# Performance work log

Hardware: AMD Instinct MI355X
Metric: run time of the kernel (lower is better)

## Reference

```python
import math
import jax, jax.numpy as jnp
import numpy as np

B, SENTS, L, S, D, DH, K = 128, 2, 2, 256, 1024, 64, 8
SCALE = math.sqrt(DH)
EPS = 1e-8


def gelu(x):
    return 0.5 * x * (1.0 + jax.lax.erf(x / np.float32(math.sqrt(2.0))))


def setup_inputs() -> dict:
    key = jax.random.key(0)
    ks = jax.random.split(key, 18)
    w = lambda k, shp: (jax.random.normal(k, shp, jnp.float32) * 0.02)
    return {
        "token": jax.random.normal(ks[0], (B, SENTS, L, S, D), jnp.float32),
        "kw_idx": jax.random.randint(ks[1], (B, SENTS, K), 0, S),
        "q_w": w(ks[2], (DH, D)), "q_b": jnp.zeros((DH,), jnp.float32),
        "k_w": w(ks[3], (DH, D)), "k_b": jnp.zeros((DH,), jnp.float32),
        "v_w": w(ks[4], (DH, D)), "v_b": jnp.zeros((DH,), jnp.float32),
        "mi_w": w(ks[5], (DH, D)), "mi_b": jnp.zeros((DH,), jnp.float32),
        "inter_w": w(ks[6], (4, DH, DH)), "inter_b": jnp.zeros((4, DH), jnp.float32),
        "fc0_w": w(ks[7], (64, 516)), "fc0_b": jnp.zeros((64,), jnp.float32),
        "fc1_w": w(ks[8], (2, 64)), "fc1_b": jnp.zeros((2,), jnp.float32),
    }


def _cosine(a, b):
    # torch.cosine_similarity semantics with eps=1e-8 (clamp each norm)
    na = jnp.maximum(jnp.linalg.norm(a, axis=1), EPS)
    nb = jnp.maximum(jnp.linalg.norm(b, axis=1), EPS)
    return jnp.sum(a * b, axis=1) / (na * nb)


def reference(token, kw_idx, q_w, q_b, k_w, k_b, v_w, v_b,
              mi_w, mi_b, inter_w, inter_b, fc0_w, fc0_b, fc1_w, fc1_b):
    b, _, l, s, d = token.shape
    kk = kw_idx.shape[-1]
    # faithful quirk: sent_id indexes keyword_idx[batch][sent_id - 1] -> swap sentences
    idx = kw_idx[:, ::-1, :]  # [B,2,K]
    # ragged gather (fixed K here): [B,2,L,K,D]
    kw = jnp.take_along_axis(token, idx[:, :, None, :, None], axis=3)
    kmax = kw.max(axis=3)   # [B,2,L,D]
    kavg = kw.mean(axis=3)  # [B,2,L,D]
    kw_flat = kw.reshape(b, 2, l * kk, d)  # layers concatenated along token axis

    q = jnp.einsum('bsnd,hd->bsnh', kw_flat, q_w) + q_b
    k = jnp.einsum('bsnd,hd->bsnh', kw_flat, k_w) + k_b
    v = jnp.einsum('bsnd,hd->bsnh', kw_flat, v_w) + v_b

    # cross-sentence attention WITHOUT softmax (as in original)
    att1 = jnp.einsum('bnh,bmh->bnm', q[:, 0], k[:, 1]) / SCALE
    e1 = jnp.einsum('bnm,bmh->bnh', att1, v[:, 1])  # [B,N,DH]
    att2 = jnp.einsum('bnh,bmh->bnm', q[:, 1], k[:, 0]) / SCALE
    e2 = jnp.einsum('bnm,bmh->bnh', att2, v[:, 0])
    att_feat = jnp.concatenate(
        [e1.max(axis=1), e1.mean(axis=1), e2.max(axis=1), e2.mean(axis=1)], axis=1)  # [B,4*DH]

    proj = lambda x: x @ mi_w.T + mi_b  # [B,D] -> [B,DH]
    s1_max = proj(kmax[:, 0].max(axis=1))
    s2_max = proj(kmax[:, 1].max(axis=1))
    s1_avg = proj(kavg[:, 0].mean(axis=1))
    s2_avg = proj(kavg[:, 1].mean(axis=1))

    inter = lambda i, x: x @ inter_w[i].T + inter_b[i]
    cos = jnp.stack([
        _cosine(inter(0, s1_max), s2_max),
        _cosine(inter(1, s1_max), s2_avg),
        _cosine(inter(2, s1_avg), s2_max),
        _cosine(inter(3, s1_avg), s2_avg),
    ], axis=1)  # [B,4]

    feature = jnp.concatenate([att_feat, cos, s1_max, s1_avg, s2_max, s2_avg], axis=1)  # [B,516]
    h = gelu(feature @ fc0_w.T + fc0_b)
    h = gelu(h @ fc1_w.T + fc1_b)
    return jax.nn.softmax(h, axis=-1)
```

## Files before the change

kernel.cpp:

```cpp
#include <hip/hip_runtime.h>
#include <math.h>

using short8 = __attribute__((ext_vector_type(8))) short;
using f32x4  = __attribute__((ext_vector_type(4))) float;

__device__ __forceinline__ short f2bf(float f) {
  union { float f; unsigned u; } cv; cv.f = f;
  unsigned u = cv.u;
  unsigned r = u + 0x7fffu + ((u >> 16) & 1u);
  return (short)(r >> 16);
}

__device__ __forceinline__ float gelu_f(float x) {
  return 0.5f * x * (1.0f + erff(x * 0.7071067811865475f));
}

__global__ void k_prep(const float* __restrict__ qw, const float* __restrict__ kw,
                       const float* __restrict__ vw, const float* __restrict__ miw,
                       const float* __restrict__ qb, const float* __restrict__ kb,
                       const float* __restrict__ vb, const float* __restrict__ mib,
                       short* __restrict__ Wb, float* __restrict__ biasc) {
  int t = blockIdx.x * 256 + threadIdx.x;
  int e = t * 4;
  int which = e >> 16;
  int off = e & 65535;
  const float* src = which == 0 ? qw : which == 1 ? kw : which == 2 ? vw : miw;
  float4 f = *reinterpret_cast<const float4*>(src + off);
  short s4[4] = { f2bf(f.x), f2bf(f.y), f2bf(f.z), f2bf(f.w) };
  *reinterpret_cast<unsigned long long*>(Wb + e) =
      *reinterpret_cast<unsigned long long*>(s4);
  if (blockIdx.x == 0) {
    int w = threadIdx.x >> 6, h = threadIdx.x & 63;
    const float* bsrc = w == 0 ? qb : w == 1 ? kb : w == 2 ? vb : mib;
    biasc[threadIdx.x] = bsrc[h];
  }
}

__global__ __launch_bounds__(256) void k_main(
    const float* __restrict__ token, const int* __restrict__ kwidx,
    const short* __restrict__ Wb, const float* __restrict__ biasc,
    float* __restrict__ qkv, float* __restrict__ svec) {
  constexpr int AS = 1032;
  __shared__ short A[18 * AS];
  const int bs = blockIdx.x;
  const int b = bs >> 1, snt = bs & 1;
  const int t = threadIdx.x;
  const int col = t * 4;
  const int* idxp = kwidx + (b * 2 + (1 - snt)) * 8;

  float mx[4], sm[4];
  #pragma unroll 4
  for (int i = 0; i < 16; ++i) {
    const int l = i >> 3, j = i & 7;
    const int sidx = idxp[j];
    const float4 f = *reinterpret_cast<const float4*>(
        token + (size_t)((bs * 2 + l) * 256 + sidx) * 1024 + col);
    float fv[4] = { f.x, f.y, f.z, f.w };
    short s4[4];
    #pragma unroll
    for (int c = 0; c < 4; ++c) {
      if (i == 0) { mx[c] = fv[c]; sm[c] = fv[c]; }
      else { mx[c] = fmaxf(mx[c], fv[c]); sm[c] += fv[c]; }
      s4[c] = f2bf(fv[c]);
    }
    *reinterpret_cast<unsigned long long*>(&A[i * AS + col]) =
        *reinterpret_cast<unsigned long long*>(s4);
  }
  {
    short pm4[4], pa4[4];
    #pragma unroll
    for (int c = 0; c < 4; ++c) { pm4[c] = f2bf(mx[c]); pa4[c] = f2bf(sm[c] * 0.0625f); }
    *reinterpret_cast<unsigned long long*>(&A[16 * AS + col]) =
        *reinterpret_cast<unsigned long long*>(pm4);
    *reinterpret_cast<unsigned long long*>(&A[17 * AS + col]) =
        *reinterpret_cast<unsigned long long*>(pa4);
  }
  __syncthreads();

  const int wave = t >> 6, lane = t & 63;
  const int quad = lane >> 4, mrow = lane & 15;
  const short* Abase = (wave == 3) ? &A[(16 + (mrow & 1)) * AS] : &A[mrow * AS];
  const short* w0 = Wb + (size_t)(wave * 64 + mrow) * 1024;

  f32x4 acc[4];
  #pragma unroll
  for (int i = 0; i < 4; ++i)
    #pragma unroll
    for (int r = 0; r < 4; ++r) acc[i][r] = 0.f;

  #pragma unroll 4
  for (int ko = 0; ko < 1024; ko += 32) {
    const int k0 = ko + quad * 8;
    short8 af = *reinterpret_cast<const short8*>(Abase + k0);
    short8 b0 = *reinterpret_cast<const short8*>(w0 + k0);
    short8 b1 = *reinterpret_cast<const short8*>(w0 + 16 * 1024 + k0);
    short8 b2 = *reinterpret_cast<const short8*>(w0 + 32 * 1024 + k0);
    short8 b3 = *reinterpret_cast<const short8*>(w0 + 48 * 1024 + k0);
    acc[0] = __builtin_amdgcn_mfma_f32_16x16x32_bf16(af, b0, acc[0], 0, 0, 0);
    acc[1] = __builtin_amdgcn_mfma_f32_16x16x32_bf16(af, b1, acc[1], 0, 0, 0);
    acc[2] = __builtin_amdgcn_mfma_f32_16x16x32_bf16(af, b2, acc[2], 0, 0, 0);
    acc[3] = __builtin_amdgcn_mfma_f32_16x16x32_bf16(af, b3, acc[3], 0, 0, 0);
  }

  const int row0 = quad * 4;
  #pragma unroll
  for (int i = 0; i < 4; ++i) {
    const int T = wave * 4 + i;
    const int hg = T * 16 + mrow;
    const float bias = biasc[hg];
    if (T < 12) {
      const int mat = hg >> 6, h = hg & 63;
      float* dst = qkv + ((size_t)(bs * 3 + mat) << 10) + h;
      #pragma unroll
      for (int r = 0; r < 4; ++r) dst[(row0 + r) * 64] = acc[i][r] + bias;
    } else {
      const int h = hg - 192;
      #pragma unroll
      for (int r = 0; r < 4; ++r) {
        const int n = row0 + r;
        if (n < 2) svec[(bs * 2 + n) * 64 + h] = acc[i][r] + bias;
      }
    }
  }
}

__global__ __launch_bounds__(256) void k_tail(
    const float* __restrict__ qkv, const float* __restrict__ svec,
    const float* __restrict__ interw, const float* __restrict__ interb,
    const float* __restrict__ fc0w, const float* __restrict__ fc0b,
    const float* __restrict__ fc1w, const float* __restrict__ fc1b,
    float* __restrict__ out) {
  const int b = blockIdx.x, t = threadIdx.x;
  __shared__ float qk[96 * 65];
  __shared__ float attL[256];
  __shared__ float eL[2][1024];
  __shared__ float feat[516];
  __shared__ float yv[256];
  __shared__ float hmid[64];
  __shared__ float red[256];

  const float* src = qkv + (size_t)b * 6144;
  for (int i = t; i < 6144; i += 256) {
    int row = i >> 6, h = i & 63;
    qk[row * 65 + h] = src[i];
  }
  feat[260 + t] = svec[b * 256 + t];
  __syncthreads();

  {
    const int n = t >> 4, m = t & 15;
    const float* qrow = &qk[n * 65];
    const float* krow = &qk[(64 + m) * 65];
    float acc = 0.f;
    for (int h = 0; h < 64; ++h) acc += qrow[h] * krow[h];
    attL[n * 16 + m] = acc * 0.125f;
  }
  __syncthreads();
  {
    const int h = t & 63, ng = t >> 6;
    for (int rep = 0; rep < 4; ++rep) {
      const int n = rep * 4 + ng;
      float acc = 0.f;
      #pragma unroll
      for (int m = 0; m < 16; ++m) acc += attL[n * 16 + m] * qk[(80 + m) * 65 + h];
      eL[0][n * 64 + h] = acc;
    }
  }
  __syncthreads();
  {
    const int n = t >> 4, m = t & 15;
    const float* qrow = &qk[(48 + n) * 65];
    const float* krow = &qk[(16 + m) * 65];
    float acc = 0.f;
    for (int h = 0; h < 64; ++h) acc += qrow[h] * krow[h];
    attL[n * 16 + m] = acc * 0.125f;
  }
  __syncthreads();
  {
    const int h = t & 63, ng = t >> 6;
    for (int rep = 0; rep < 4; ++rep) {
      const int n = rep * 4 + ng;
      float acc = 0.f;
      #pragma unroll
      for (int m = 0; m < 16; ++m) acc += attL[n * 16 + m] * qk[(32 + m) * 65 + h];
      eL[1][n * 64 + h] = acc;
    }
  }
  __syncthreads();
  {
    const int stat = t >> 6, h = t & 63;
    const float* ee = eL[stat >> 1];
    float r;
    if ((stat & 1) == 0) {
      r = -INFINITY;
      for (int n = 0; n < 16; ++n) r = fmaxf(r, ee[n * 64 + h]);
    } else {
      r = 0.f;
      for (int n = 0; n < 16; ++n) r += ee[n * 64 + h];
      r *= (1.f / 16.f);
    }
    feat[stat * 64 + h] = r;
  }
  __syncthreads();
  {
    const int i = t >> 6, h = t & 63;
    const float* x = (i < 2) ? &feat[260] : &feat[324];
    const float* wrow = interw + (i * 64 + h) * 64;
    float acc = interb[i * 64 + h];
    for (int hp = 0; hp < 64; ++hp) acc += x[hp] * wrow[hp];
    yv[i * 64 + h] = acc;
  }
  __syncthreads();
  if (t < 4) {
    const float* y = &yv[t * 64];
    const float* z = (t & 1) ? &feat[452] : &feat[388];
    float dy = 0.f, ny = 0.f, nz = 0.f;
    for (int h = 0; h < 64; ++h) { dy += y[h] * z[h]; ny += y[h] * y[h]; nz += z[h] * z[h]; }
    float na = fmaxf(sqrtf(ny), 1e-8f), nb = fmaxf(sqrtf(nz), 1e-8f);
    feat[256 + t] = dy / (na * nb);
  }
  __syncthreads();
  {
    const int o = t & 63, part = t >> 6;
    const int f0 = part * 129;
    const float* wrow = fc0w + o * 516;
    float acc = 0.f;
    for (int f = f0; f < f0 + 129; ++f) acc += feat[f] * wrow[f];
    red[t] = acc;
  }
  __syncthreads();
  if (t < 64) {
    float acc = fc0b[t] + red[t] + red[64 + t] + red[128 + t] + red[192 + t];
    hmid[t] = gelu_f(acc);
  }
  __syncthreads();
  if (t == 0) {
    float lg[2];
    for (int c = 0; c < 2; ++c) {
      float acc = fc1b[c];
      for (int o = 0; o < 64; ++o) acc += hmid[o] * fc1w[c * 64 + o];
      lg[c] = gelu_f(acc);
    }
    const float mxv = fmaxf(lg[0], lg[1]);
    const float e0 = expf(lg[0] - mxv), e1v = expf(lg[1] - mxv);
    out[b * 2]     = e0 / (e0 + e1v);
    out[b * 2 + 1] = e1v / (e0 + e1v);
  }
}

extern "C" void kernel_launch(void* const* d_in, const int* in_sizes, int n_in,
                              void* d_out, int out_size, void* d_ws, size_t ws_size,
                              hipStream_t stream) {
  (void)in_sizes; (void)n_in; (void)out_size; (void)ws_size;
  const float* token  = (const float*)d_in[0];
  const int*   kwidx  = (const int*)d_in[1];
  const float* qw     = (const float*)d_in[2];
  const float* qb     = (const float*)d_in[3];
  const float* kw     = (const float*)d_in[4];
  const float* kb     = (const float*)d_in[5];
  const float* vw     = (const float*)d_in[6];
  const float* vb     = (const float*)d_in[7];
  const float* miw    = (const float*)d_in[8];
  const float* mib    = (const float*)d_in[9];
  const float* interw = (const float*)d_in[10];
  const float* interb = (const float*)d_in[11];
  const float* fc0w   = (const float*)d_in[12];
  const float* fc0b   = (const float*)d_in[13];
  const float* fc1w   = (const float*)d_in[14];
  const float* fc1b   = (const float*)d_in[15];
  float* out = (float*)d_out;

  char* ws = (char*)d_ws;
  short* Wb    = (short*)(ws);
  float* biasc = (float*)(ws + 524288);
  float* qkv   = (float*)(ws + 525312);
  float* svec  = (float*)(ws + 3671040);

  k_prep<<<256, 256, 0, stream>>>(qw, kw, vw, miw, qb, kb, vb, mib, Wb, biasc);
  k_main<<<256, 256, 0, stream>>>(token, kwidx, Wb, biasc, qkv, svec);
  k_tail<<<128, 256, 0, stream>>>(qkv, svec, interw, interb, fc0w, fc0b, fc1w, fc1b, out);
}
```

Baseline: 629.4 us.

## Quadruple k_main threads with one MFMA tile per wave; coalesce tail matvecs

k_main now launches 1024 threads per block. The keyword-row gather is split across four row groups, and each of the 16 waves computes a single 16-column MFMA output tile instead of four. The goal is more memory and compute parallelism per block, since the grid has only 256 blocks. Max and mean are now computed from the bf16-rounded values held in shared memory, which slightly changes numerics and adds a barrier. In k_tail, the inter projection and fc0 layers are rewritten so lanes read weight rows contiguously and reduce with wave shuffles, replacing strided per-thread row reads.

Result: slower. 676.7 us (+7.5%).

```diff
diff --git a/kernel.cpp b/kernel.cpp
--- a/kernel.cpp
+++ b/kernel.cpp
@@ -10,7 +10,11 @@
   unsigned r = u + 0x7fffu + ((u >> 16) & 1u);
   return (short)(r >> 16);
 }
-
+__device__ __forceinline__ float bf2f(short s) {
+  union { unsigned u; float f; } cv;
+  cv.u = ((unsigned)(unsigned short)s) << 16;
+  return cv.f;
+}
 __device__ __forceinline__ float gelu_f(float x) {
   return 0.5f * x * (1.0f + erff(x * 0.7071067811865475f));
 }
@@ -36,7 +40,7 @@
   }
 }
 
-__global__ __launch_bounds__(256) void k_main(
+__global__ __launch_bounds__(1024) void k_main(
     const float* __restrict__ token, const int* __restrict__ kwidx,
     const short* __restrict__ Wb, const float* __restrict__ biasc,
     float* __restrict__ qkv, float* __restrict__ svec) {
@@ -45,81 +49,74 @@
   const int bs = blockIdx.x;
   const int b = bs >> 1, snt = bs & 1;
   const int t = threadIdx.x;
-  const int col = t * 4;
   const int* idxp = kwidx + (b * 2 + (1 - snt)) * 8;
 
-  float mx[4], sm[4];
-  #pragma unroll 4
-  for (int i = 0; i < 16; ++i) {
-    const int l = i >> 3, j = i & 7;
-    const int sidx = idxp[j];
-    const float4 f = *reinterpret_cast<const float4*>(
-        token + (size_t)((bs * 2 + l) * 256 + sidx) * 1024 + col);
-    float fv[4] = { f.x, f.y, f.z, f.w };
-    short s4[4];
-    #pragma unroll
-    for (int c = 0; c < 4; ++c) {
-      if (i == 0) { mx[c] = fv[c]; sm[c] = fv[c]; }
-      else { mx[c] = fmaxf(mx[c], fv[c]); sm[c] += fv[c]; }
-      s4[c] = f2bf(fv[c]);
-    }
-    *reinterpret_cast<unsigned long long*>(&A[i * AS + col]) =
-        *reinterpret_cast<unsigned long long*>(s4);
-  }
-  {
+  {
+    const int cc = (t & 255) * 4;
+    const int r0 = (t >> 8) * 4;
+    #pragma unroll
+    for (int i = r0; i < r0 + 4; ++i) {
+      const int l = i >> 3, j = i & 7;
+      const int sidx = idxp[j];
+      const float4 f = *reinterpret_cast<const float4*>(
+          token + (size_t)((bs * 2 + l) * 256 + sidx) * 1024 + cc);
+      short s4[4] = { f2bf(f.x), f2bf(f.y), f2bf(f.z), f2bf(f.w) };
+      *reinterpret_cast<unsigned long long*>(&A[i * AS + cc]) =
+          *reinterpret_cast<unsigned long long*>(s4);
+    }
+  }
+  __syncthreads();
+  if (t < 256) {
+    const int cc = t * 4;
+    float mx[4], sm[4];
+    #pragma unroll
+    for (int i = 0; i < 16; ++i) {
+      unsigned long long v = *reinterpret_cast<unsigned long long*>(&A[i * AS + cc]);
+      #pragma unroll
+      for (int c = 0; c < 4; ++c) {
+        float f = bf2f((short)(v >> (16 * c)));
+        if (i == 0) { mx[c] = f; sm[c] = f; }
+        else { mx[c] = fmaxf(mx[c], f); sm[c] += f; }
+      }
+    }
     short pm4[4], pa4[4];
     #pragma unroll
     for (int c = 0; c < 4; ++c) { pm4[c] = f2bf(mx[c]); pa4[c] = f2bf(sm[c] * 0.0625f); }
-    *reinterpret_cast<unsigned long long*>(&A[16 * AS + col]) =
+    *reinterpret_cast<unsigned long long*>(&A[16 * AS + cc]) =
         *reinterpret_cast<unsigned long long*>(pm4);
-    *reinterpret_cast<unsigned long long*>(&A[17 * AS + col]) =
+    *reinterpret_cast<unsigned long long*>(&A[17 * AS + cc]) =
         *reinterpret_cast<unsigned long long*>(pa4);
   }
   __syncthreads();
 
   const int wave = t >> 6, lane = t & 63;
   const int quad = lane >> 4, mrow = lane & 15;
-  const short* Abase = (wave == 3) ? &A[(16 + (mrow & 1)) * AS] : &A[mrow * AS];
-  const short* w0 = Wb + (size_t)(wave * 64 + mrow) * 1024;
-
-  f32x4 acc[4];
-  #pragma unroll
-  for (int i = 0; i < 4; ++i)
-    #pragma unroll
-    for (int r = 0; r < 4; ++r) acc[i][r] = 0.f;
-
-  #pragma unroll 4
+  const short* Abase = (wave >= 12) ? &A[(16 + (mrow & 1)) * AS] : &A[mrow * AS];
+  const short* w0 = Wb + (size_t)(wave * 16 + mrow) * 1024;
+
+  f32x4 acc = { 0.f, 0.f, 0.f, 0.f };
+  #pragma unroll 8
   for (int ko = 0; ko < 1024; ko += 32) {
     const int k0 = ko + quad * 8;
     short8 af = *reinterpret_cast<const short8*>(Abase + k0);
-    short8 b0 = *reinterpret_cast<const short8*>(w0 + k0);
-    short8 b1 = *reinterpret_cast<const short8*>(w0 + 16 * 1024 + k0);
-    short8 b2 = *reinterpret_cast<const short8*>(w0 + 32 * 1024 + k0);
-    short8 b3 = *reinterpret_cast<const short8*>(w0 + 48 * 1024 + k0);
-    acc[0] = __builtin_amdgcn_mfma_f32_16x16x32_bf16(af, b0, acc[0], 0, 0, 0);
-    acc[1] = __builtin_amdgcn_mfma_f32_16x16x32_bf16(af, b1, acc[1], 0, 0, 0);
-    acc[2] = __builtin_amdgcn_mfma_f32_16x16x32_bf16(af, b2, acc[2], 0, 0, 0);
-    acc[3] = __builtin_amdgcn_mfma_f32_16x16x32_bf16(af, b3, acc[3], 0, 0, 0);
-  }
-
+    short8 bf = *reinterpret_cast<const short8*>(w0 + k0);
+    acc = __builtin_amdgcn_mfma_f32_16x16x32_bf16(af, bf, acc, 0, 0, 0);
+  }
+
+  const int hg = wave * 16 + mrow;
+  const float bias = biasc[hg];
   const int row0 = quad * 4;
-  #pragma unroll
-  for (int i = 0; i < 4; ++i) {
-    const int T = wave * 4 + i;
-    const int hg = T * 16 + mrow;
-    const float bias = biasc[hg];
-    if (T < 12) {
-      const int mat = hg >> 6, h = hg & 63;
-      float* dst = qkv + ((size_t)(bs * 3 + mat) << 10) + h;
-      #pragma unroll
-      for (int r = 0; r < 4; ++r) dst[(row0 + r) * 64] = acc[i][r] + bias;
-    } else {
-      const int h = hg - 192;
-      #pragma unroll
-      for (int r = 0; r < 4; ++r) {
-        const int n = row0 + r;
-        if (n < 2) svec[(bs * 2 + n) * 64 + h] = acc[i][r] + bias;
-      }
+  if (wave < 12) {
+    const int mat = hg >> 6, h = hg & 63;
+    float* dst = qkv + ((size_t)(bs * 3 + mat) << 10) + h;
+    #pragma unroll
+    for (int r = 0; r < 4; ++r) dst[(row0 + r) * 64] = acc[r] + bias;
+  } else {
+    const int h = hg - 192;
+    #pragma unroll
+    for (int r = 0; r < 4; ++r) {
+      const int n = row0 + r;
+      if (n < 2) svec[(bs * 2 + n) * 64 + h] = acc[r] + bias;
     }
   }
 }
@@ -131,13 +128,13 @@
     const float* __restrict__ fc1w, const float* __restrict__ fc1b,
     float* __restrict__ out) {
   const int b = blockIdx.x, t = threadIdx.x;
+  const int wave = t >> 6, lane = t & 63;
   __shared__ float qk[96 * 65];
   __shared__ float attL[256];
   __shared__ float eL[2][1024];
   __shared__ float feat[516];
   __shared__ float yv[256];
   __shared__ float hmid[64];
-  __shared__ float red[256];
 
   const float* src = qkv + (size_t)b * 6144;
   for (int i = t; i < 6144; i += 256) {
@@ -203,12 +200,14 @@
   }
   __syncthreads();
   {
-    const int i = t >> 6, h = t & 63;
-    const float* x = (i < 2) ? &feat[260] : &feat[324];
-    const float* wrow = interw + (i * 64 + h) * 64;
-    float acc = interb[i * 64 + h];
-    for (int hp = 0; hp < 64; ++hp) acc += x[hp] * wrow[hp];
-    yv[i * 64 + h] = acc;
+    const float xl = feat[260 + ((wave >> 1) ? 64 : 0) + lane];
+    const float* wbase = interw + wave * 4096;
+    for (int o = 0; o < 64; ++o) {
+      float p = xl * wbase[o * 64 + lane];
+      #pragma unroll
+      for (int s = 32; s; s >>= 1) p += __shfl_xor(p, s);
+      if (lane == o) yv[wave * 64 + o] = p + interb[wave * 64 + o];
+    }
   }
   __syncthreads();
   if (t < 4) {
@@ -221,17 +220,22 @@
   }
   __syncthreads();
   {
-    const int o = t & 63, part = t >> 6;
-    const int f0 = part * 129;
-    const float* wrow = fc0w + o * 516;
-    float acc = 0.f;
-    for (int f = f0; f < f0 + 129; ++f) acc += feat[f] * wrow[f];
-    red[t] = acc;
-  }
-  __syncthreads();
-  if (t < 64) {
-    float acc = fc0b[t] + red[t] + red[64 + t] + red[128 + t] + red[192 + t];
-    hmid[t] = gelu_f(acc);
+    float fv[9];
+    #pragma unroll
+    for (int c = 0; c < 9; ++c) {
+      const int f = c * 64 + lane;
+      fv[c] = (f < 516) ? feat[f] : 0.f;
+    }
+    for (int r = 0; r < 16; ++r) {
+      const int o = wave * 16 + r;
+      const float* wrow = fc0w + o * 516;
+      float p = (lane < 4) ? fv[8] * wrow[512 + lane] : 0.f;
+      #pragma unroll
+      for (int c = 0; c < 8; ++c) p += fv[c] * wrow[c * 64 + lane];
+      #pragma unroll
+      for (int s = 32; s; s >>= 1) p += __shfl_xor(p, s);
+      if (lane == 0) hmid[o] = gelu_f(p + fc0b[o]);
+    }
   }
   __syncthreads();
   if (t == 0) {
@@ -277,6 +281,6 @@
   float* svec  = (float*)(ws + 3671040);
 
   k_prep<<<256, 256, 0, stream>>>(qw, kw, vw, miw, qb, kb, vb, mib, Wb, biasc);
-  k_main<<<256, 256, 0, stream>>>(token, kwidx, Wb, biasc, qkv, svec);
+  k_main<<<256, 1024, 0, stream>>>(token, kwidx, Wb, biasc, qkv, svec);
   k_tail<<<128, 256, 0, stream>>>(qkv, svec, interw, interb, fc0w, fc0b, fc1w, fc1b, out);
 }
```
